# Kernel tuning notes

Hardware: AMD Instinct MI355X
Metric: run time of the kernel (lower is better)

Reference implementation:

```python
import jax, jax.numpy as jnp
import numpy as np

C = 64          # n_channels
NCLS = 10       # output_size
EPS = 1e-5      # GroupNorm eps (torch default)
T0, DT, NSTEPS = 0.0, 0.1, 10  # t0=0, t1=1, dt=0.1 -> 10 fixed RK4 steps


def _gn(x, w, b):
    # GroupNorm(C, C): per-sample, per-channel norm over H,W
    m = x.mean(axis=(2, 3), keepdims=True)
    v = ((x - m) ** 2).mean(axis=(2, 3), keepdims=True)
    return (x - m) * jax.lax.rsqrt(v + EPS) * w[None, :, None, None] + b[None, :, None, None]


def _conv(x, w, b, stride, pad):
    y = jax.lax.conv_general_dilated(x, w, (stride, stride), pad,
                                     dimension_numbers=('NCHW', 'OIHW', 'NCHW'))
    return y + b[None, :, None, None]


def setup_inputs() -> dict:
    key = jax.random.key(0)
    ks = jax.random.split(key, 8)
    rnd = lambda k, shape, s: jax.random.normal(k, shape, jnp.float32) * s
    B = 64
    return dict(
        x=jax.random.normal(ks[0], (B, 1, 130, 130), jnp.float32),
        # downsampler: Conv(1->C,3,1,VALID), GN, ReLU, Conv(C->C,4,2,1), GN, ReLU, Conv(C->C,4,2,1)
        ds_w1=rnd(ks[1], (C, 1, 3, 3), 0.2), ds_b1=jnp.zeros((C,), jnp.float32),
        ds_n1w=jnp.ones((C,), jnp.float32), ds_n1b=jnp.zeros((C,), jnp.float32),
        ds_w2=rnd(ks[2], (C, C, 4, 4), 0.03), ds_b2=jnp.zeros((C,), jnp.float32),
        ds_n2w=jnp.ones((C,), jnp.float32), ds_n2b=jnp.zeros((C,), jnp.float32),
        ds_w3=rnd(ks[3], (C, C, 4, 4), 0.03), ds_b3=jnp.zeros((C,), jnp.float32),
        # ODE RHS: two Conv2d(C+1 -> C, 3, 1, 1) with time channel concat, two GroupNorms
        ode_w1=rnd(ks[4], (C, C + 1, 3, 3), 0.04), ode_b1=jnp.zeros((C,), jnp.float32),
        ode_n1w=jnp.ones((C,), jnp.float32), ode_n1b=jnp.zeros((C,), jnp.float32),
        ode_w2=rnd(ks[5], (C, C + 1, 3, 3), 0.04), ode_b2=jnp.zeros((C,), jnp.float32),
        ode_n2w=jnp.ones((C,), jnp.float32), ode_n2b=jnp.zeros((C,), jnp.float32),
        # classification head: GN, ReLU, GAP, Linear(C -> 10)
        head_nw=jnp.ones((C,), jnp.float32), head_nb=jnp.zeros((C,), jnp.float32),
        head_W=rnd(ks[6], (NCLS, C), 0.1), head_b=jnp.zeros((NCLS,), jnp.float32),
    )


def reference(x, ds_w1, ds_b1, ds_n1w, ds_n1b, ds_w2, ds_b2, ds_n2w, ds_n2b, ds_w3, ds_b3,
              ode_w1, ode_b1, ode_n1w, ode_n1b, ode_w2, ode_b2, ode_n2w, ode_n2b,
              head_nw, head_nb, head_W, head_b):
    P1 = [(1, 1), (1, 1)]
    # ---- downsampler ----
    h = _conv(x, ds_w1, ds_b1, 1, 'VALID')                      # [B,C,128,128]
    h = jax.nn.relu(_gn(h, ds_n1w, ds_n1b))
    h = _conv(h, ds_w2, ds_b2, 2, P1)                           # [B,C,64,64]
    h = jax.nn.relu(_gn(h, ds_n2w, ds_n2b))
    h = _conv(h, ds_w3, ds_b3, 2, P1)                           # [B,C,32,32]

    # ---- ODE layer: fixed-step classic RK4 (tableau_low), 10 steps ----
    def rhs(t, z):
        z = jax.nn.relu(_gn(z, ode_n1w, ode_n1b))
        ts = jnp.full_like(z[:, :1], t)
        z = _conv(jnp.concatenate((ts, z), axis=1), ode_w1, ode_b1, 1, P1)
        z = jax.nn.relu(_gn(z, ode_n2w, ode_n2b))
        ts = jnp.full_like(z[:, :1], t)
        z = _conv(jnp.concatenate((ts, z), axis=1), ode_w2, ode_b2, 1, P1)
        return z

    def step(z, i):
        t = T0 + i * DT
        k1 = rhs(t, z)
        k2 = rhs(t + 0.5 * DT, z + 0.5 * DT * k1)
        k3 = rhs(t + 0.5 * DT, z + 0.5 * DT * k2)
        k4 = rhs(t + DT, z + DT * k3)
        return z + (DT / 6.0) * (k1 + 2.0 * k2 + 2.0 * k3 + k4), None

    h, _ = jax.lax.scan(step, h, jnp.arange(NSTEPS, dtype=jnp.float32))

    # ---- classification head ----
    h = jax.nn.relu(_gn(h, head_nw, head_nb))
    h = h.mean(axis=(2, 3))                                     # AdaptiveAvgPool2d((1,1)) + Flatten
    return h @ head_W.T + head_b                                # [B, 10]
```

## Files before the change

### kernel.cpp

```cpp
#include <hip/hip_runtime.h>

#define BB 64
#define CC 64

typedef __attribute__((ext_vector_type(8))) short short8;
typedef __attribute__((ext_vector_type(4))) short short4v;
typedef __attribute__((ext_vector_type(4))) float f32x4;

__device__ __forceinline__ float bf2f(unsigned short h) {
    unsigned int u = ((unsigned int)h) << 16;
    float f; __builtin_memcpy(&f, &u, 4); return f;
}
__device__ __forceinline__ unsigned short f2bf(float f) {
    unsigned int u; __builtin_memcpy(&u, &f, 4);
    u += 0x7fffu + ((u >> 16) & 1u);
    return (unsigned short)(u >> 16);
}

__global__ __launch_bounds__(256) void conv1stats_kernel(const float* __restrict__ x,
    const float* __restrict__ w1, const float* __restrict__ b1,
    float* __restrict__ ps, float* __restrict__ ps2) {
    __shared__ float sw1[576];
    __shared__ float sb1[64];
    __shared__ float xs[10 * 130];
    int tid = threadIdx.x;
    int qq = blockIdx.x;
    int b = blockIdx.y;
    for (int i = tid; i < 576; i += 256) sw1[i] = w1[i];
    if (tid < 64) sb1[tid] = b1[tid];
    const float* xb = x + (size_t)b * 130 * 130;
    int c = tid >> 2, q = tid & 3;
    float s = 0.f, s2 = 0.f;
    for (int sidx = 0; sidx < 2; sidx++) {
        int row0 = (qq * 2 + sidx) * 8;
        __syncthreads();
        for (int i = tid; i < 1300; i += 256) xs[i] = xb[row0 * 130 + i];
        __syncthreads();
        const float* wc = &sw1[c * 9];
        float bc = sb1[c];
        for (int p = q; p < 1024; p += 4) {
            int y = p >> 7, xx = p & 127;
            float v = bc;
#pragma unroll
            for (int ky = 0; ky < 3; ky++)
#pragma unroll
                for (int kx = 0; kx < 3; kx++)
                    v += xs[(y + ky) * 130 + xx + kx] * wc[ky * 3 + kx];
            s += v; s2 += v * v;
        }
    }
    s  += __shfl_xor(s, 1, 64);  s  += __shfl_xor(s, 2, 64);
    s2 += __shfl_xor(s2, 1, 64); s2 += __shfl_xor(s2, 2, 64);
    if (q == 0) {
        ps [(b * 8 + qq) * 64 + c] = s;
        ps2[(b * 8 + qq) * 64 + c] = s2;
    }
}

__global__ __launch_bounds__(256) void gn1fin_kernel(const float* __restrict__ ps,
    const float* __restrict__ ps2, const float* __restrict__ n1w, const float* __restrict__ n1b,
    float* __restrict__ gn1sc, float* __restrict__ gn1sh) {
    int i = blockIdx.x * 256 + threadIdx.x;
    if (i >= BB * CC) return;
    int c = i & 63, b = i >> 6;
    float s = 0.f, s2 = 0.f;
#pragma unroll
    for (int qq = 0; qq < 8; qq++) {
        s  += ps [(b * 8 + qq) * 64 + c];
        s2 += ps2[(b * 8 + qq) * 64 + c];
    }
    float mean = s / 16384.f;
    float var = s2 / 16384.f - mean * mean;
    float rstd = rsqrtf(var + 1e-5f);
    float sc = rstd * n1w[c];
    gn1sc[i] = sc;
    gn1sh[i] = n1b[c] - mean * sc;
}

__global__ __launch_bounds__(256) void prepack_kernel(const float* __restrict__ w1,
    const float* __restrict__ w2, const float* __restrict__ dw2,
    const float* __restrict__ dw3, unsigned short* __restrict__ Apk,
    float* __restrict__ Stab) {
    int set = blockIdx.y, kc = blockIdx.x, tid = threadIdx.x;
    int nchunk = (set < 2) ? 18 : 32;
    if (kc < nchunk) {
        const float* w = (set == 0) ? w1 : (set == 1) ? w2 : (set == 2) ? dw2 : dw3;
        size_t off = (set == 0) ? 0 : (set == 1) ? 36864 : (set == 2) ? 73728 : 139264;
        for (int e = tid; e < 2048; e += 256) {
            int co = e >> 5, j = e & 31;
            int k = kc * 32 + j;
            int ci = k & 63;
            int tap = k >> 6;
            float val;
            if (set < 2) val = w[(co * 65 + ci + 1) * 9 + tap];
            else         val = w[((co << 6) + ci) * 16 + tap];
            Apk[off + (size_t)kc * 2048 + e] = f2bf(val);
        }
    }
    if (set < 2 && kc == 0) {
        const float* w = set ? w2 : w1;
        for (int t = tid; t < 576; t += 256) {
            int co = t / 9, tap = t % 9;
            Stab[set * 576 + t] = w[(co * 65) * 9 + tap];
        }
    }
}

__global__ __launch_bounds__(256) void ds2mfma_kernel(const float* __restrict__ x,
    const float* __restrict__ w1, const float* __restrict__ b1,
    const float* __restrict__ gn1sc, const float* __restrict__ gn1sh,
    const unsigned short* __restrict__ Apk, const float* __restrict__ bias2,
    unsigned short* __restrict__ h2, float* __restrict__ sums_out) {
    __shared__ unsigned short X[2 * 198 * 64];
    __shared__ float xs[8 * 68];
    __shared__ float sw1[576];
    __shared__ float sb1[64], ssc[64], ssh[64], sb2[64];
    __shared__ float sred[4][64], s2red[4][64];
    int tid = threadIdx.x;
    int b = blockIdx.y;
    int bx = blockIdx.x;
    int xh = bx & 1, sy = bx >> 1;
    int lane = tid & 63, w = tid >> 6;
    int colL = lane & 15, quad = lane >> 4;

    for (int i = tid; i < 576; i += 256) sw1[i] = w1[i];
    if (tid < 64) {
        sb1[tid] = b1[tid];
        ssc[tid] = gn1sc[b * 64 + tid];
        ssh[tid] = gn1sh[b * 64 + tid];
        sb2[tid] = bias2[tid];
    }
    {
        const float* xb = x + (size_t)b * 130 * 130;
        for (int i = tid; i < 544; i += 256) {
            int r = i / 68, cc = i % 68;
            int xr = 4 * sy - 1 + r, xcg = 64 * xh - 1 + cc;
            xs[i] = (xr >= 0 && xr < 130 && xcg >= 0 && xcg < 130) ? xb[xr * 130 + xcg] : 0.f;
        }
    }
    __syncthreads();
    {
        int sub = tid & 7;
        float sbr[8], scr[8], shr[8];
#pragma unroll
        for (int e = 0; e < 8; e++) {
            int c = sub * 8 + e;
            sbr[e] = sb1[c]; scr[e] = ssc[c]; shr[e] = ssh[c];
        }
        for (int i = tid; i < 3168; i += 256) {
            int pidx = i >> 3;
            int ir = pidx / 66, ic = pidx - ir * 66;
            int gy = 4 * sy - 1 + ir, gxg = 64 * xh - 1 + ic;
            short8 o;
            if (gy >= 0 && gy < 128 && gxg >= 0 && gxg < 128) {
#pragma unroll
                for (int e = 0; e < 8; e++) {
                    int c = sub * 8 + e;
                    float v = sbr[e];
#pragma unroll
                    for (int ky = 0; ky < 3; ky++)
#pragma unroll
                        for (int kx = 0; kx < 3; kx++)
                            v += xs[(ir + ky) * 68 + ic + kx] * sw1[c * 9 + ky * 3 + kx];
                    o[e] = (short)f2bf(fmaxf(fmaf(v, scr[e], shr[e]), 0.f));
                }
            } else {
#pragma unroll
                for (int e = 0; e < 8; e++) o[e] = 0;
            }
            int p = ic & 1;
            int psx = ir * 33 + (ic >> 1);
            *(short8*)(X + ((p * 198 + psx) << 6) + ((sub ^ (psx & 7)) << 3)) = o;
        }
    }
    __syncthreads();

    int l = w >> 1, oxb = (w & 1) * 16;
    int oxl = oxb + colL;
    f32x4 acc[4] = {};
    for (int kc = 0; kc < 32; ++kc) {
        int tap = kc >> 1;
        int ky = tap >> 2, kx = tap & 3;
        int chgrp = (kc & 1) * 4 + quad;
        int ir = 2 * l + ky;
        int p = kx & 1;
        int psx = ir * 33 + oxl + (kx >> 1);
        short8 bb = *(const short8*)(X + ((p * 198 + psx) << 6) + ((chgrp ^ (psx & 7)) << 3));
        const unsigned short* ap = Apk + (((kc << 6) + colL) << 5) + (quad << 3);
        short8 a0 = *(const short8*)(ap);
        short8 a1 = *(const short8*)(ap + 512);
        short8 a2 = *(const short8*)(ap + 1024);
        short8 a3 = *(const short8*)(ap + 1536);
        acc[0] = __builtin_amdgcn_mfma_f32_16x16x32_bf16(a0, bb, acc[0], 0, 0, 0);
        acc[1] = __builtin_amdgcn_mfma_f32_16x16x32_bf16(a1, bb, acc[1], 0, 0, 0);
        acc[2] = __builtin_amdgcn_mfma_f32_16x16x32_bf16(a2, bb, acc[2], 0, 0, 0);
        acc[3] = __builtin_amdgcn_mfma_f32_16x16x32_bf16(a3, bb, acc[3], 0, 0, 0);
    }

    float sl[16], s2l[16];
#pragma unroll
    for (int i = 0; i < 16; i++) { sl[i] = 0.f; s2l[i] = 0.f; }
    int oy = 2 * sy + l, oxg = xh * 32 + oxl;
#pragma unroll
    for (int mt = 0; mt < 4; ++mt) {
        int co0 = mt * 16 + quad * 4;
        size_t base = ((size_t)((b * 64 + oy) * 64 + oxg)) * 64 + co0;
        short4v o;
#pragma unroll
        for (int r = 0; r < 4; ++r) {
            unsigned short hh = f2bf(acc[mt][r] + sb2[co0 + r]);
            o[r] = (short)hh;
            float f = bf2f(hh);
            sl[mt * 4 + r] += f; s2l[mt * 4 + r] += f * f;
        }
        *(short4v*)(h2 + base) = o;
    }
#pragma unroll
    for (int idx = 0; idx < 16; ++idx) {
        float s = sl[idx], s2 = s2l[idx];
        s += __shfl_xor(s, 1, 64); s += __shfl_xor(s, 2, 64);
        s += __shfl_xor(s, 4, 64); s += __shfl_xor(s, 8, 64);
        s2 += __shfl_xor(s2, 1, 64); s2 += __shfl_xor(s2, 2, 64);
        s2 += __shfl_xor(s2, 4, 64); s2 += __shfl_xor(s2, 8, 64);
        if (colL == 0) {
            int co = (idx >> 2) * 16 + quad * 4 + (idx & 3);
            sred[w][co] = s; s2red[w][co] = s2;
        }
    }
    __syncthreads();
    if (tid < 64) {
        float s = sred[0][tid] + sred[1][tid] + sred[2][tid] + sred[3][tid];
        float s2 = s2red[0][tid] + s2red[1][tid] + s2red[2][tid] + s2red[3][tid];
        atomicAdd(&sums_out[b * 64 + tid], s);
        atomicAdd(&sums_out[4096 + b * 64 + tid], s2);
    }
}

__global__ __launch_bounds__(256) void ds3mfma_kernel(const unsigned short* __restrict__ h2,
    const float* __restrict__ sums_in, const float* __restrict__ gw, const float* __restrict__ gb,
    const unsigned short* __restrict__ Apk, const float* __restrict__ bias3,
    float* __restrict__ z, unsigned short* __restrict__ zb, float* __restrict__ sums_out) {
    __shared__ unsigned short X[2 * 198 * 64];
    __shared__ float ssc[64], ssh[64], sb3[64];
    __shared__ float sred[4][64], s2red[4][64];
    int tid = threadIdx.x;
    int b = blockIdx.y, sy = blockIdx.x;
    int lane = tid & 63, w = tid >> 6;
    int colL = lane & 15, quad = lane >> 4;

    if (tid < 64) {
        int c = tid;
        float s = sums_in[b * 64 + c];
        float s2 = sums_in[4096 + b * 64 + c];
        float mean = s * (1.f / 4096.f);
        float var = fmaxf(s2 * (1.f / 4096.f) - mean * mean, 0.f);
        float sc = rsqrtf(var + 1e-5f) * gw[c];
        ssc[c] = sc;
        ssh[c] = gb[c] - mean * sc;
        sb3[c] = bias3[c];
    }
    __syncthreads();
    {
        int sub = tid & 7;
        float scr[8], shr[8];
#pragma unroll
        for (int e = 0; e < 8; e++) { scr[e] = ssc[sub * 8 + e]; shr[e] = ssh[sub * 8 + e]; }
        for (int i = tid; i < 3168; i += 256) {
            int pidx = i >> 3;
            int ir = pidx / 66, ic = pidx - ir * 66;
            int gy = 4 * sy - 1 + ir, gx = ic - 1;
            short8 o;
            if (gy >= 0 && gy < 64 && gx >= 0 && gx < 64) {
                short8 d = *(const short8*)(h2 + ((size_t)((b * 64 + gy) * 64 + gx)) * 64 + sub * 8);
#pragma unroll
                for (int e = 0; e < 8; e++) {
                    float f = bf2f((unsigned short)d[e]);
                    o[e] = (short)f2bf(fmaxf(fmaf(f, scr[e], shr[e]), 0.f));
                }
            } else {
#pragma unroll
                for (int e = 0; e < 8; e++) o[e] = 0;
            }
            int p = ic & 1;
            int psx = ir * 33 + (ic >> 1);
            *(short8*)(X + ((p * 198 + psx) << 6) + ((sub ^ (psx & 7)) << 3)) = o;
        }
    }
    __syncthreads();

    int l = w >> 1, oxb = (w & 1) * 16;
    int oxl = oxb + colL;
    f32x4 acc[4] = {};
    for (int kc = 0; kc < 32; ++kc) {
        int tap = kc >> 1;
        int ky = tap >> 2, kx = tap & 3;
        int chgrp = (kc & 1) * 4 + quad;
        int ir = 2 * l + ky;
        int p = kx & 1;
        int psx = ir * 33 + oxl + (kx >> 1);
        short8 bb = *(const short8*)(X + ((p * 198 + psx) << 6) + ((chgrp ^ (psx & 7)) << 3));
        const unsigned short* ap = Apk + (((kc << 6) + colL) << 5) + (quad << 3);
        short8 a0 = *(const short8*)(ap);
        short8 a1 = *(const short8*)(ap + 512);
        short8 a2 = *(const short8*)(ap + 1024);
        short8 a3 = *(const short8*)(ap + 1536);
        acc[0] = __builtin_amdgcn_mfma_f32_16x16x32_bf16(a0, bb, acc[0], 0, 0, 0);
        acc[1] = __builtin_amdgcn_mfma_f32_16x16x32_bf16(a1, bb, acc[1], 0, 0, 0);
        acc[2] = __builtin_amdgcn_mfma_f32_16x16x32_bf16(a2, bb, acc[2], 0, 0, 0);
        acc[3] = __builtin_amdgcn_mfma_f32_16x16x32_bf16(a3, bb, acc[3], 0, 0, 0);
    }

    float sl[16], s2l[16];
#pragma unroll
    for (int i = 0; i < 16; i++) { sl[i] = 0.f; s2l[i] = 0.f; }
    int py = 2 * sy + l;
#pragma unroll
    for (int mt = 0; mt < 4; ++mt) {
        int co0 = mt * 16 + quad * 4;
        size_t base = ((size_t)((b << 10) + py * 32 + oxl)) * 64 + co0;
        f32x4 zv;
        short4v o;
#pragma unroll
        for (int r = 0; r < 4; ++r) {
            float val = acc[mt][r] + sb3[co0 + r];
            zv[r] = val;
            unsigned short hh = f2bf(val);
            o[r] = (short)hh;
            float f = bf2f(hh);
            sl[mt * 4 + r] += f; s2l[mt * 4 + r] += f * f;
        }
        *(f32x4*)(z + base) = zv;
        *(short4v*)(zb + base) = o;
    }
#pragma unroll
    for (int idx = 0; idx < 16; ++idx) {
        float s = sl[idx], s2 = s2l[idx];
        s += __shfl_xor(s, 1, 64); s += __shfl_xor(s, 2, 64);
        s += __shfl_xor(s, 4, 64); s += __shfl_xor(s, 8, 64);
        s2 += __shfl_xor(s2, 1, 64); s2 += __shfl_xor(s2, 2, 64);
        s2 += __shfl_xor(s2, 4, 64); s2 += __shfl_xor(s2, 8, 64);
        if (colL == 0) {
            int co = (idx >> 2) * 16 + quad * 4 + (idx & 3);
            sred[w][co] = s; s2red[w][co] = s2;
        }
    }
    __syncthreads();
    if (tid < 64) {
        float s = sred[0][tid] + sred[1][tid] + sred[2][tid] + sred[3][tid];
        float s2 = s2red[0][tid] + s2red[1][tid] + s2red[2][tid] + s2red[3][tid];
        atomicAdd(&sums_out[b * 64 + tid], s);
        atomicAdd(&sums_out[4096 + b * 64 + tid], s2);
    }
}

__global__ __launch_bounds__(256) void convmfma_kernel(
    const unsigned short* __restrict__ uin, const float* __restrict__ sums_in,
    const float* __restrict__ gw, const float* __restrict__ gb,
    const unsigned short* __restrict__ Apk, const float* __restrict__ stab,
    const float* __restrict__ bias, float t, float aa, int mode,
    float* __restrict__ z, unsigned short* __restrict__ uout,
    float* __restrict__ kacc, float* __restrict__ sums_out)
{
    __shared__ unsigned short X[6 * 34 * 64];
    __shared__ float ssc[64], ssh[64];
    __shared__ float tS[64], trow0[64], trow2[64], tcol0[64], tcol2[64];
    __shared__ float tc00[64], tc02[64], tc20[64], tc22[64];
    __shared__ float sred[4][64], s2red[4][64];

    int tid = threadIdx.x;
    int b = blockIdx.y, strip = blockIdx.x;
    int y0 = strip * 4;
    int lane = tid & 63, w = tid >> 6;
    int colL = lane & 15, quad = lane >> 4;

    {
        f32x4 zz = 0.f;
        for (int i = tid; i < 1632; i += 256) ((f32x4*)X)[i] = zz;
    }
    if (tid < 64) {
        int c = tid;
        float s = sums_in[b * 64 + c];
        float s2 = sums_in[4096 + b * 64 + c];
        float mean = s * (1.f / 1024.f);
        float var = fmaxf(s2 * (1.f / 1024.f) - mean * mean, 0.f);
        float sc = rsqrtf(var + 1e-5f) * gw[c];
        ssc[c] = sc;
        ssh[c] = gb[c] - mean * sc;
    } else if (tid < 128) {
        int co = tid - 64;
        float w0[9];
#pragma unroll
        for (int k = 0; k < 9; k++) w0[k] = stab[co * 9 + k] * t;
        tS[co] = bias[co] + w0[0]+w0[1]+w0[2]+w0[3]+w0[4]+w0[5]+w0[6]+w0[7]+w0[8];
        trow0[co] = w0[0] + w0[1] + w0[2];
        trow2[co] = w0[6] + w0[7] + w0[8];
        tcol0[co] = w0[0] + w0[3] + w0[6];
        tcol2[co] = w0[2] + w0[5] + w0[8];
        tc00[co] = w0[0]; tc02[co] = w0[2]; tc20[co] = w0[6]; tc22[co] = w0[8];
    }
    __syncthreads();

    {
        int sub = tid & 7;
        float scr[8], shr[8];
#pragma unroll
        for (int e = 0; e < 8; e++) { scr[e] = ssc[sub * 8 + e]; shr[e] = ssh[sub * 8 + e]; }
#pragma unroll
        for (int it = 0; it < 6; ++it) {
            int i = tid + it * 256;
            int pidx = i >> 3;
            int xc = pidx & 31, r = pidx >> 5;
            int gy = y0 - 1 + r;
            if (gy < 0 || gy > 31) continue;
            int gp = (b << 10) + gy * 32 + xc;
            short8 d = *(const short8*)(uin + (size_t)gp * 64 + sub * 8);
            short8 o;
#pragma unroll
            for (int e = 0; e < 8; e++) {
                float f = bf2f((unsigned short)d[e]);
                o[e] = (short)f2bf(fmaxf(fmaf(f, scr[e], shr[e]), 0.f));
            }
            int psx = r * 34 + xc + 1;
            *(short8*)(X + (psx << 6) + ((sub ^ (psx & 7)) << 3)) = o;
        }
    }
    __syncthreads();

    f32x4 acc[4][2] = {};
    for (int kc = 0; kc < 18; ++kc) {
        int tap = kc >> 1;
        int dy = tap / 3, dx = tap % 3;
        int chgrp = (kc & 1) * 4 + quad;
        int ps0 = (w + dy) * 34 + colL + dx;
        int ps1 = ps0 + 16;
        short8 bb0 = *(const short8*)(X + (ps0 << 6) + ((chgrp ^ (ps0 & 7)) << 3));
        short8 bb1 = *(const short8*)(X + (ps1 << 6) + ((chgrp ^ (ps1 & 7)) << 3));
        const unsigned short* ap = Apk + (((kc << 6) + colL) << 5) + (quad << 3);
        short8 a0 = *(const short8*)(ap);
        short8 a1 = *(const short8*)(ap + 512);
        short8 a2 = *(const short8*)(ap + 1024);
        short8 a3 = *(const short8*)(ap + 1536);
        acc[0][0] = __builtin_amdgcn_mfma_f32_16x16x32_bf16(a0, bb0, acc[0][0], 0, 0, 0);
        acc[0][1] = __builtin_amdgcn_mfma_f32_16x16x32_bf16(a0, bb1, acc[0][1], 0, 0, 0);
        acc[1][0] = __builtin_amdgcn_mfma_f32_16x16x32_bf16(a1, bb0, acc[1][0], 0, 0, 0);
        acc[1][1] = __builtin_amdgcn_mfma_f32_16x16x32_bf16(a1, bb1, acc[1][1], 0, 0, 0);
        acc[2][0] = __builtin_amdgcn_mfma_f32_16x16x32_bf16(a2, bb0, acc[2][0], 0, 0, 0);
        acc[2][1] = __builtin_amdgcn_mfma_f32_16x16x32_bf16(a2, bb1, acc[2][1], 0, 0, 0);
        acc[3][0] = __builtin_amdgcn_mfma_f32_16x16x32_bf16(a3, bb0, acc[3][0], 0, 0, 0);
        acc[3][1] = __builtin_amdgcn_mfma_f32_16x16x32_bf16(a3, bb1, acc[3][1], 0, 0, 0);
    }

    float sl[16], s2l[16];
#pragma unroll
    for (int i = 0; i < 16; i++) { sl[i] = 0.f; s2l[i] = 0.f; }
    int py = y0 + w;
    bool by0 = (py == 0), by1 = (py == 31);
#pragma unroll
    for (int nt = 0; nt < 2; ++nt) {
        int px = nt * 16 + colL;
        bool bx0 = (px == 0), bx1 = (px == 31);
#pragma unroll
        for (int mt = 0; mt < 4; ++mt) {
            int co0 = mt * 16 + quad * 4;
            float vout[4];
#pragma unroll
            for (int r = 0; r < 4; ++r) {
                int co = co0 + r;
                float val = acc[mt][nt][r] + tS[co];
                if (by0) { val -= trow0[co]; if (bx0) val += tc00[co]; if (bx1) val += tc02[co]; }
                if (by1) { val -= trow2[co]; if (bx0) val += tc20[co]; if (bx1) val += tc22[co]; }
                if (bx0) val -= tcol0[co];
                if (bx1) val -= tcol2[co];
                vout[r] = val;
            }
            size_t base = ((size_t)((b << 10) + py * 32 + px)) * 64 + co0;
            if (mode == 3) {
                short4v o;
#pragma unroll
                for (int r = 0; r < 4; ++r) {
                    unsigned short hh = f2bf(vout[r]);
                    o[r] = (short)hh;
                    float f = bf2f(hh);
                    sl[mt * 4 + r] += f; s2l[mt * 4 + r] += f * f;
                }
                *(short4v*)(uout + base) = o;
            } else if (mode == 2) {
                f32x4 kv = *(const f32x4*)(kacc + base);
                f32x4 zv = *(const f32x4*)(z + base);
                short4v o;
#pragma unroll
                for (int r = 0; r < 4; ++r) {
                    float zn = zv[r] + aa * (kv[r] + vout[r]);
                    zv[r] = zn;
                    unsigned short hh = f2bf(zn);
                    o[r] = (short)hh;
                    float f = bf2f(hh);
                    sl[mt * 4 + r] += f; s2l[mt * 4 + r] += f * f;
                }
                *(f32x4*)(z + base) = zv;
                *(short4v*)(uout + base) = o;
            } else {
                f32x4 zv = *(const f32x4*)(z + base);
                f32x4 kv;
                if (mode == 1) {
                    kv = *(const f32x4*)(kacc + base);
#pragma unroll
                    for (int r = 0; r < 4; ++r) kv[r] += 2.f * vout[r];
                } else {
#pragma unroll
                    for (int r = 0; r < 4; ++r) kv[r] = vout[r];
                }
                *(f32x4*)(kacc + base) = kv;
                short4v o;
#pragma unroll
                for (int r = 0; r < 4; ++r) {
                    unsigned short hh = f2bf(zv[r] + aa * vout[r]);
                    o[r] = (short)hh;
                    float f = bf2f(hh);
                    sl[mt * 4 + r] += f; s2l[mt * 4 + r] += f * f;
                }
                *(short4v*)(uout + base) = o;
            }
        }
    }
#pragma unroll
    for (int idx = 0; idx < 16; ++idx) {
        float s = sl[idx], s2 = s2l[idx];
        s += __shfl_xor(s, 1, 64); s += __shfl_xor(s, 2, 64);
        s += __shfl_xor(s, 4, 64); s += __shfl_xor(s, 8, 64);
        s2 += __shfl_xor(s2, 1, 64); s2 += __shfl_xor(s2, 2, 64);
        s2 += __shfl_xor(s2, 4, 64); s2 += __shfl_xor(s2, 8, 64);
        if (colL == 0) {
            int co = (idx >> 2) * 16 + quad * 4 + (idx & 3);
            sred[w][co] = s; s2red[w][co] = s2;
        }
    }
    __syncthreads();
    if (tid < 64) {
        float s = sred[0][tid] + sred[1][tid] + sred[2][tid] + sred[3][tid];
        float s2 = s2red[0][tid] + s2red[1][tid] + s2red[2][tid] + s2red[3][tid];
        atomicAdd(&sums_out[b * 64 + tid], s);
        atomicAdd(&sums_out[4096 + b * 64 + tid], s2);
    }
}

__global__ __launch_bounds__(256) void headgap_kernel(const float* __restrict__ z,
    const float* __restrict__ w, const float* __restrict__ b, float* __restrict__ pooled) {
    __shared__ float r1[4][64], r2[4][64];
    __shared__ float scs[64], shs[64];
    int bq = blockIdx.x, tid = threadIdx.x;
    int c = tid & 63, g = tid >> 6;
    float s = 0.f, s2 = 0.f;
    for (int p = g; p < 1024; p += 4) {
        float v = z[((size_t)((bq << 10) + p)) * 64 + c];
        s += v; s2 += v * v;
    }
    r1[g][c] = s; r2[g][c] = s2;
    __syncthreads();
    if (tid < 64) {
        float ts = r1[0][tid] + r1[1][tid] + r1[2][tid] + r1[3][tid];
        float ts2 = r2[0][tid] + r2[1][tid] + r2[2][tid] + r2[3][tid];
        float mean = ts / 1024.f;
        float var = fmaxf(ts2 / 1024.f - mean * mean, 0.f);
        float sc = rsqrtf(var + 1e-5f) * w[tid];
        scs[tid] = sc;
        shs[tid] = b[tid] - mean * sc;
    }
    __syncthreads();
    float sc = scs[c], sh = shs[c];
    float r = 0.f;
    for (int p = g; p < 1024; p += 4)
        r += fmaxf(fmaf(z[((size_t)((bq << 10) + p)) * 64 + c], sc, sh), 0.f);
    r1[g][c] = r;
    __syncthreads();
    if (tid < 64)
        pooled[bq * 64 + tid] = (r1[0][tid] + r1[1][tid] + r1[2][tid] + r1[3][tid]) / 1024.f;
}

__global__ __launch_bounds__(256) void headfc_kernel(const float* __restrict__ pooled,
    const float* __restrict__ W, const float* __restrict__ bias, float* __restrict__ out) {
    int i = blockIdx.x * 256 + threadIdx.x;
    if (i < 640) {
        int b = i / 10, j = i % 10;
        float a = bias[j];
        const float* p = pooled + b * 64;
        const float* wj = W + j * 64;
#pragma unroll 8
        for (int c = 0; c < 64; c++) a += p[c] * wj[c];
        out[i] = a;
    }
}

extern "C" void kernel_launch(void* const* d_in, const int* in_sizes, int n_in,
                              void* d_out, int out_size, void* d_ws, size_t ws_size,
                              hipStream_t stream) {
    const float* x      = (const float*)d_in[0];
    const float* ds_w1  = (const float*)d_in[1];
    const float* ds_b1  = (const float*)d_in[2];
    const float* ds_n1w = (const float*)d_in[3];
    const float* ds_n1b = (const float*)d_in[4];
    const float* ds_w2  = (const float*)d_in[5];
    const float* ds_b2  = (const float*)d_in[6];
    const float* ds_n2w = (const float*)d_in[7];
    const float* ds_n2b = (const float*)d_in[8];
    const float* ds_w3  = (const float*)d_in[9];
    const float* ds_b3  = (const float*)d_in[10];
    const float* ode_w1 = (const float*)d_in[11];
    const float* ode_b1 = (const float*)d_in[12];
    const float* ode_n1w= (const float*)d_in[13];
    const float* ode_n1b= (const float*)d_in[14];
    const float* ode_w2 = (const float*)d_in[15];
    const float* ode_b2 = (const float*)d_in[16];
    const float* ode_n2w= (const float*)d_in[17];
    const float* ode_n2b= (const float*)d_in[18];
    const float* head_nw= (const float*)d_in[19];
    const float* head_nb= (const float*)d_in[20];
    const float* head_W = (const float*)d_in[21];
    const float* head_b = (const float*)d_in[22];

    const size_t NZ = (size_t)BB * CC * 32 * 32;
    float* ws = (float*)d_ws;
    float*          z     = ws;
    unsigned short* zb    = (unsigned short*)(ws + NZ);
    unsigned short* u     = (unsigned short*)(ws + 3 * NZ / 2);
    unsigned short* v     = (unsigned short*)(ws + 2 * NZ);
    float*          kacc  = ws + 5 * NZ / 2;
    unsigned short* h2    = u;
    float*          apf   = ws + 7 * NZ / 2;
    unsigned short* Apk   = (unsigned short*)apf;
    float*          Stab  = apf + 102400;
    float*          sums  = Stab + 1152;
    float*          ps    = sums + 82 * 8192;
    float*          ps2   = ps + 32768;
    float*          gn1sc = ps2 + 32768;
    float*          gn1sh = gn1sc + 4096;
    float*          pooled= gn1sh + 4096;

    auto SUM = [&](int s) { return sums + (size_t)s * 8192; };
    auto SV = [&](int i, int j) { return 1 + i * 7 + j; };
    auto SU = [&](int i, int j) { return 1 + i * 7 + 4 + j; };
    auto ZS = [&](int i) { return 71 + i; };
    const int H2S = 81;

    hipMemsetAsync(sums, 0, 82 * 8192 * sizeof(float), stream);
    prepack_kernel<<<dim3(32, 4), 256, 0, stream>>>(ode_w1, ode_w2, ds_w2, ds_w3, Apk, Stab);

    conv1stats_kernel<<<dim3(8, BB), 256, 0, stream>>>(x, ds_w1, ds_b1, ps, ps2);
    gn1fin_kernel<<<16, 256, 0, stream>>>(ps, ps2, ds_n1w, ds_n1b, gn1sc, gn1sh);
    ds2mfma_kernel<<<dim3(64, BB), 256, 0, stream>>>(x, ds_w1, ds_b1, gn1sc, gn1sh,
        Apk + 73728, ds_b2, h2, SUM(H2S));
    ds3mfma_kernel<<<dim3(16, BB), 256, 0, stream>>>(h2, SUM(H2S), ds_n2w, ds_n2b,
        Apk + 139264, ds_b3, z, zb, SUM(0));

    const unsigned short* AP1 = Apk;
    const unsigned short* AP2 = Apk + 36864;
    const float* ST1 = Stab;
    const float* ST2 = Stab + 576;
    const float c6 = 0.1f / 6.0f;
    dim3 cgrid(8, BB);
    for (int i = 0; i < 10; i++) {
        float t0 = 0.1f * (float)i;
        int zslot = (i == 0) ? 0 : ZS(i - 1);
        convmfma_kernel<<<cgrid, 256, 0, stream>>>(zb, SUM(zslot), ode_n1w, ode_n1b,
            AP1, ST1, ode_b1, t0, 0.f, 3, z, v, kacc, SUM(SV(i, 0)));
        convmfma_kernel<<<cgrid, 256, 0, stream>>>(v, SUM(SV(i, 0)), ode_n2w, ode_n2b,
            AP2, ST2, ode_b2, t0, 0.05f, 0, z, u, kacc, SUM(SU(i, 0)));
        convmfma_kernel<<<cgrid, 256, 0, stream>>>(u, SUM(SU(i, 0)), ode_n1w, ode_n1b,
            AP1, ST1, ode_b1, t0 + 0.05f, 0.f, 3, z, v, kacc, SUM(SV(i, 1)));
        convmfma_kernel<<<cgrid, 256, 0, stream>>>(v, SUM(SV(i, 1)), ode_n2w, ode_n2b,
            AP2, ST2, ode_b2, t0 + 0.05f, 0.05f, 1, z, u, kacc, SUM(SU(i, 1)));
        convmfma_kernel<<<cgrid, 256, 0, stream>>>(u, SUM(SU(i, 1)), ode_n1w, ode_n1b,
            AP1, ST1, ode_b1, t0 + 0.05f, 0.f, 3, z, v, kacc, SUM(SV(i, 2)));
        convmfma_kernel<<<cgrid, 256, 0, stream>>>(v, SUM(SV(i, 2)), ode_n2w, ode_n2b,
            AP2, ST2, ode_b2, t0 + 0.05f, 0.1f, 1, z, u, kacc, SUM(SU(i, 2)));
        convmfma_kernel<<<cgrid, 256, 0, stream>>>(u, SUM(SU(i, 2)), ode_n1w, ode_n1b,
            AP1, ST1, ode_b1, t0 + 0.1f, 0.f, 3, z, v, kacc, SUM(SV(i, 3)));
        convmfma_kernel<<<cgrid, 256, 0, stream>>>(v, SUM(SV(i, 3)), ode_n2w, ode_n2b,
            AP2, ST2, ode_b2, t0 + 0.1f, c6, 2, z, zb, kacc, SUM(ZS(i)));
    }

    headgap_kernel<<<BB, 256, 0, stream>>>(z, head_nw, head_nb, pooled);
    headfc_kernel<<<3, 256, 0, stream>>>(pooled, head_W, head_b, (float*)d_out);
}
```

Measured before the change: 2.597 ms.

## Stage conv weights in LDS and double rows per 512-thread block

The ODE conv kernel now copies its packed bf16 weight matrix (about 73 KB) into dynamic shared memory once per block. The MFMA loop then reads A operands from LDS instead of global memory. Each block grows to 512 threads covering 8 output rows, halving the grid, so every weight copy is reused across twice as many pixels and the halo overhead per row drops. In exchange, each block needs about 124 KB of LDS, which limits residency to one block per CU. It also adds a serial weight-copy prologue before any compute starts.

```diff
diff --git a/kernel.cpp b/kernel.cpp
--- a/kernel.cpp
+++ b/kernel.cpp
@@ -353,7 +353,8 @@
     }
 }
 
-__global__ __launch_bounds__(256) void convmfma_kernel(
+#define CONV_LDS_BYTES 124416
+__global__ __launch_bounds__(512, 2) void convmfma_kernel(
     const unsigned short* __restrict__ uin, const float* __restrict__ sums_in,
     const float* __restrict__ gw, const float* __restrict__ gb,
     const unsigned short* __restrict__ Apk, const float* __restrict__ stab,
@@ -361,22 +362,30 @@
     float* __restrict__ z, unsigned short* __restrict__ uout,
     float* __restrict__ kacc, float* __restrict__ sums_out)
 {
-    __shared__ unsigned short X[6 * 34 * 64];
-    __shared__ float ssc[64], ssh[64];
-    __shared__ float tS[64], trow0[64], trow2[64], tcol0[64], tcol2[64];
-    __shared__ float tc00[64], tc02[64], tc20[64], tc22[64];
-    __shared__ float sred[4][64], s2red[4][64];
+    extern __shared__ unsigned short smem[];
+    unsigned short* Aw = smem;
+    unsigned short* X  = smem + 36864;
+    float* fp    = (float*)(smem + 36864 + 21760);
+    float* ssc   = fp;        float* ssh   = fp + 64;
+    float* tS    = fp + 128;  float* trow0 = fp + 192;  float* trow2 = fp + 256;
+    float* tcol0 = fp + 320;  float* tcol2 = fp + 384;
+    float* tc00  = fp + 448;  float* tc02  = fp + 512;
+    float* tc20  = fp + 576;  float* tc22  = fp + 640;
+    float* sred  = fp + 704;
+    float* s2red = fp + 1216;
 
     int tid = threadIdx.x;
     int b = blockIdx.y, strip = blockIdx.x;
-    int y0 = strip * 4;
+    int y0 = strip * 8;
     int lane = tid & 63, w = tid >> 6;
     int colL = lane & 15, quad = lane >> 4;
 
     {
         f32x4 zz = 0.f;
-        for (int i = tid; i < 1632; i += 256) ((f32x4*)X)[i] = zz;
-    }
+        for (int i = tid; i < 2720; i += 512) ((f32x4*)X)[i] = zz;
+    }
+    for (int i = tid; i < 4608; i += 512) ((f32x4*)Aw)[i] = ((const f32x4*)Apk)[i];
+
     if (tid < 64) {
         int c = tid;
         float s = sums_in[b * 64 + c];
@@ -406,10 +415,9 @@
 #pragma unroll
         for (int e = 0; e < 8; e++) { scr[e] = ssc[sub * 8 + e]; shr[e] = ssh[sub * 8 + e]; }
 #pragma unroll
-        for (int it = 0; it < 6; ++it) {
-            int i = tid + it * 256;
-            int pidx = i >> 3;
-            int xc = pidx & 31, r = pidx >> 5;
+        for (int it = 0; it < 5; ++it) {
+            int pidx = (tid >> 3) + it * 64;
+            int r = pidx >> 5, xc = pidx & 31;
             int gy = y0 - 1 + r;
             if (gy < 0 || gy > 31) continue;
             int gp = (b << 10) + gy * 32 + xc;
@@ -435,7 +443,7 @@
         int ps1 = ps0 + 16;
         short8 bb0 = *(const short8*)(X + (ps0 << 6) + ((chgrp ^ (ps0 & 7)) << 3));
         short8 bb1 = *(const short8*)(X + (ps1 << 6) + ((chgrp ^ (ps1 & 7)) << 3));
-        const unsigned short* ap = Apk + (((kc << 6) + colL) << 5) + (quad << 3);
+        const unsigned short* ap = Aw + (((kc << 6) + colL) << 5) + (quad << 3);
         short8 a0 = *(const short8*)(ap);
         short8 a1 = *(const short8*)(ap + 512);
         short8 a2 = *(const short8*)(ap + 1024);
@@ -532,13 +540,14 @@
         s2 += __shfl_xor(s2, 4, 64); s2 += __shfl_xor(s2, 8, 64);
         if (colL == 0) {
             int co = (idx >> 2) * 16 + quad * 4 + (idx & 3);
-            sred[w][co] = s; s2red[w][co] = s2;
+            sred[w * 64 + co] = s; s2red[w * 64 + co] = s2;
         }
     }
     __syncthreads();
     if (tid < 64) {
-        float s = sred[0][tid] + sred[1][tid] + sred[2][tid] + sred[3][tid];
-        float s2 = s2red[0][tid] + s2red[1][tid] + s2red[2][tid] + s2red[3][tid];
+        float s = 0.f, s2 = 0.f;
+#pragma unroll
+        for (int i = 0; i < 8; i++) { s += sred[i * 64 + tid]; s2 += s2red[i * 64 + tid]; }
         atomicAdd(&sums_out[b * 64 + tid], s);
         atomicAdd(&sums_out[4096 + b * 64 + tid], s2);
     }
@@ -642,6 +651,9 @@
     auto ZS = [&](int i) { return 71 + i; };
     const int H2S = 81;
 
+    hipFuncSetAttribute(reinterpret_cast<const void*>(convmfma_kernel),
+                        hipFuncAttributeMaxDynamicSharedMemorySize, CONV_LDS_BYTES);
+
     hipMemsetAsync(sums, 0, 82 * 8192 * sizeof(float), stream);
     prepack_kernel<<<dim3(32, 4), 256, 0, stream>>>(ode_w1, ode_w2, ds_w2, ds_w3, Apk, Stab);
 
@@ -657,25 +669,25 @@
     const float* ST1 = Stab;
     const float* ST2 = Stab + 576;
     const float c6 = 0.1f / 6.0f;
-    dim3 cgrid(8, BB);
+    dim3 cgrid(4, BB);
     for (int i = 0; i < 10; i++) {
         float t0 = 0.1f * (float)i;
         int zslot = (i == 0) ? 0 : ZS(i - 1);
-        convmfma_kernel<<<cgrid, 256, 0, stream>>>(zb, SUM(zslot), ode_n1w, ode_n1b,
+        convmfma_kernel<<<cgrid, 512, CONV_LDS_BYTES, stream>>>(zb, SUM(zslot), ode_n1w, ode_n1b,
             AP1, ST1, ode_b1, t0, 0.f, 3, z, v, kacc, SUM(SV(i, 0)));
-        convmfma_kernel<<<cgrid, 256, 0, stream>>>(v, SUM(SV(i, 0)), ode_n2w, ode_n2b,
+        convmfma_kernel<<<cgrid, 512, CONV_LDS_BYTES, stream>>>(v, SUM(SV(i, 0)), ode_n2w, ode_n2b,
             AP2, ST2, ode_b2, t0, 0.05f, 0, z, u, kacc, SUM(SU(i, 0)));
-        convmfma_kernel<<<cgrid, 256, 0, stream>>>(u, SUM(SU(i, 0)), ode_n1w, ode_n1b,
+        convmfma_kernel<<<cgrid, 512, CONV_LDS_BYTES, stream>>>(u, SUM(SU(i, 0)), ode_n1w, ode_n1b,
             AP1, ST1, ode_b1, t0 + 0.05f, 0.f, 3, z, v, kacc, SUM(SV(i, 1)));
-        convmfma_kernel<<<cgrid, 256, 0, stream>>>(v, SUM(SV(i, 1)), ode_n2w, ode_n2b,
+        convmfma_kernel<<<cgrid, 512, CONV_LDS_BYTES, stream>>>(v, SUM(SV(i, 1)), ode_n2w, ode_n2b,
             AP2, ST2, ode_b2, t0 + 0.05f, 0.05f, 1, z, u, kacc, SUM(SU(i, 1)));
-        convmfma_kernel<<<cgrid, 256, 0, stream>>>(u, SUM(SU(i, 1)), ode_n1w, ode_n1b,
+        convmfma_kernel<<<cgrid, 512, CONV_LDS_BYTES, stream>>>(u, SUM(SU(i, 1)), ode_n1w, ode_n1b,
             AP1, ST1, ode_b1, t0 + 0.05f, 0.f, 3, z, v, kacc, SUM(SV(i, 2)));
-        convmfma_kernel<<<cgrid, 256, 0, stream>>>(v, SUM(SV(i, 2)), ode_n2w, ode_n2b,
+        convmfma_kernel<<<cgrid, 512, CONV_LDS_BYTES, stream>>>(v, SUM(SV(i, 2)), ode_n2w, ode_n2b,
             AP2, ST2, ode_b2, t0 + 0.05f, 0.1f, 1, z, u, kacc, SUM(SU(i, 2)));
-        convmfma_kernel<<<cgrid, 256, 0, stream>>>(u, SUM(SU(i, 2)), ode_n1w, ode_n1b,
+        convmfma_kernel<<<cgrid, 512, CONV_LDS_BYTES, stream>>>(u, SUM(SU(i, 2)), ode_n1w, ode_n1b,
             AP1, ST1, ode_b1, t0 + 0.1f, 0.f, 3, z, v, kacc, SUM(SV(i, 3)));
-        convmfma_kernel<<<cgrid, 256, 0, stream>>>(v, SUM(SV(i, 3)), ode_n2w, ode_n2b,
+        convmfma_kernel<<<cgrid, 512, CONV_LDS_BYTES, stream>>>(v, SUM(SV(i, 3)), ode_n2w, ode_n2b,
             AP2, ST2, ode_b2, t0 + 0.1f, c6, 2, z, zb, kacc, SUM(ZS(i)));
     }
 
```

Measured after the change: 2.250 ms. -13.4%, faster.
